# Performance work log

Measured on AMD Instinct MI355X. Metric: run time of the kernel, lower is better.

## Reference

```python
import math
import jax, jax.numpy as jnp
import numpy as np

B, S, D, H, DFF, MEM = 4, 1024, 1024, 16, 4096, 256
HD = D // H  # 64
EPS = 1e-5


def _ln(x, g, b):
    mu = jnp.mean(x, axis=-1, keepdims=True)
    var = jnp.mean(jnp.square(x - mu), axis=-1, keepdims=True)
    return (x - mu) * jax.lax.rsqrt(var + EPS) * g + b


def _rope(x, cos, sin):
    # x: (b, h, s, hd); cos/sin: (>=s, hd//2)
    s = x.shape[2]
    xp = x.reshape(*x.shape[:-1], -1, 2)
    x0, x1 = xp[..., 0], xp[..., 1]
    c = cos[:s][None, None]
    sn = sin[:s][None, None]
    r0 = x0 * c - x1 * sn
    r1 = x0 * sn + x1 * c
    return jnp.stack([r0, r1], axis=-1).reshape(x.shape)


def setup_inputs() -> dict:
    key = jax.random.key(0)
    ks = jax.random.split(key, 16)
    p = lambda k, shape: jax.random.normal(k, shape, dtype=jnp.float32) * 0.02

    tgt = jax.random.normal(ks[0], (B, S, D), dtype=jnp.float32)
    memory = jax.random.normal(ks[1], (B, MEM, D), dtype=jnp.float32)

    # causal additive mask (s, s)
    tgt_mask = jnp.where(jnp.tril(jnp.ones((S, S), bool)), 0.0, -1e9).astype(jnp.float32)

    # RoPE freqs, theta=10000
    inv_freq = 1.0 / (10000.0 ** (np.arange(0, HD, 2, dtype=np.float32) / HD))
    ang = np.arange(S, dtype=np.float32)[:, None] * inv_freq[None, :]
    rope_cos = jnp.asarray(np.cos(ang))
    rope_sin = jnp.asarray(np.sin(ang))

    return {
        "tgt": tgt, "memory": memory, "tgt_mask": tgt_mask,
        "rope_cos": rope_cos, "rope_sin": rope_sin,
        "qkv_w": p(ks[2], (3 * D, D)), "qkv_b": jnp.zeros((3 * D,), jnp.float32),
        "out_w": p(ks[3], (D, D)), "out_b": jnp.zeros((D,), jnp.float32),
        "ca_in_w": p(ks[4], (3 * D, D)), "ca_in_b": jnp.zeros((3 * D,), jnp.float32),
        "ca_out_w": p(ks[5], (D, D)), "ca_out_b": jnp.zeros((D,), jnp.float32),
        "ffn_w1": p(ks[6], (DFF, D)), "ffn_b1": jnp.zeros((DFF,), jnp.float32),
        "ffn_w2": p(ks[7], (D, DFF)), "ffn_b2": jnp.zeros((D,), jnp.float32),
        "ln1_g": jnp.ones((D,), jnp.float32), "ln1_b": jnp.zeros((D,), jnp.float32),
        "ln2_g": jnp.ones((D,), jnp.float32), "ln2_b": jnp.zeros((D,), jnp.float32),
        "ln3_g": jnp.ones((D,), jnp.float32), "ln3_b": jnp.zeros((D,), jnp.float32),
    }


def reference(tgt, memory, tgt_mask, rope_cos, rope_sin,
              qkv_w, qkv_b, out_w, out_b,
              ca_in_w, ca_in_b, ca_out_w, ca_out_b,
              ffn_w1, ffn_b1, ffn_w2, ffn_b2,
              ln1_g, ln1_b, ln2_g, ln2_b, ln3_g, ln3_b):
    b, s, d = tgt.shape
    scale = 1.0 / math.sqrt(HD)

    # ---- self-attention with RoPE ----
    x = _ln(tgt, ln1_g, ln1_b)
    qkv = (x @ qkv_w.T + qkv_b).reshape(b, s, 3, H, HD)
    qkv = jnp.transpose(qkv, (2, 0, 3, 1, 4))  # (3, b, h, s, hd)
    q, k, v = qkv[0], qkv[1], qkv[2]
    q = _rope(q, rope_cos, rope_sin)
    k = _rope(k, rope_cos, rope_sin)
    attn = jnp.einsum('bhqd,bhkd->bhqk', q, k) * scale
    attn = attn + tgt_mask[None, None]
    attn = jax.nn.softmax(attn, axis=-1)
    sa = jnp.einsum('bhqk,bhkd->bhqd', attn, v)
    sa = jnp.transpose(sa, (0, 2, 1, 3)).reshape(b, s, d)
    tgt = tgt + (sa @ out_w.T + out_b)

    # ---- cross-attention (standard MHA, no positional encoding) ----
    x = _ln(tgt, ln2_g, ln2_b)
    wq, wk, wv = jnp.split(ca_in_w, 3, axis=0)
    bq, bk, bv = jnp.split(ca_in_b, 3, axis=0)
    m = memory.shape[1]
    cq = (x @ wq.T + bq).reshape(b, s, H, HD).transpose(0, 2, 1, 3)
    ck = (memory @ wk.T + bk).reshape(b, m, H, HD).transpose(0, 2, 1, 3)
    cv = (memory @ wv.T + bv).reshape(b, m, H, HD).transpose(0, 2, 1, 3)
    cattn = jax.nn.softmax(jnp.einsum('bhqd,bhkd->bhqk', cq, ck) * scale, axis=-1)
    co = jnp.einsum('bhqk,bhkd->bhqd', cattn, cv)
    co = jnp.transpose(co, (0, 2, 1, 3)).reshape(b, s, d)
    tgt = tgt + (co @ ca_out_w.T + ca_out_b)

    # ---- FFN (exact GELU, as torch nn.GELU default) ----
    x = _ln(tgt, ln3_g, ln3_b)
    ff = jax.nn.gelu(x @ ffn_w1.T + ffn_b1, approximate=False) @ ffn_w2.T + ffn_b2
    return tgt + ff
```

## Files before the change

kernel.cpp:

```cpp
#include <hip/hip_runtime.h>
#include <hip/hip_bf16.h>


using bf16 = __hip_bfloat16;
typedef __bf16 bf16x8 __attribute__((ext_vector_type(8)));
typedef float f32x4 __attribute__((ext_vector_type(4)));

static constexpr int Bn = 4, Ssz = 1024, Dm = 1024, Hh = 16, HDd = 64, DFFn = 4096, MEMn = 256;

__device__ inline float bf2f(bf16 x) { return __bfloat162float(x); }
__device__ inline bf16 f2bf(float x) { return __float2bfloat16(x); }

__global__ void detect_kernel(const unsigned* __restrict__ cosw, int* __restrict__ flag) {
  if (threadIdx.x == 0) *flag = (cosw[0] == 0x3F800000u) ? 1 : 0;
}

struct CanonArgs {
  const void* src[23];
  void* dst[23];
  int n[23];
};
__global__ __launch_bounds__(256) void canon_all(CanonArgs a, float* __restrict__ resid,
                                                 const int* __restrict__ flagp) {
  const int seg = blockIdx.y;
  const int n4 = a.n[seg] >> 2;
  if (n4 == 0) return;
  const int fl = *flagp;
  if (fl) {
    const float4* s = (const float4*)a.src[seg];
    bf16* d = (bf16*)a.dst[seg];
    for (int i = blockIdx.x * 256 + threadIdx.x; i < n4; i += gridDim.x * 256) {
      float4 v = s[i];
      bf16 t[4] = {f2bf(v.x), f2bf(v.y), f2bf(v.z), f2bf(v.w)};
      *reinterpret_cast<unsigned long long*>(d + i * 4) =
          *reinterpret_cast<unsigned long long*>(t);
      if (seg == 0) *reinterpret_cast<float4*>(resid + i * 4) = v;
    }
  } else {
    const unsigned long long* s = (const unsigned long long*)a.src[seg];
    unsigned long long* d = (unsigned long long*)a.dst[seg];
    for (int i = blockIdx.x * 256 + threadIdx.x; i < n4; i += gridDim.x * 256) {
      unsigned long long v = s[i];
      d[i] = v;
      if (seg == 0) {
        const unsigned short* u = reinterpret_cast<const unsigned short*>(&v);
        float4 f;
        f.x = __uint_as_float(((unsigned)u[0]) << 16);
        f.y = __uint_as_float(((unsigned)u[1]) << 16);
        f.z = __uint_as_float(((unsigned)u[2]) << 16);
        f.w = __uint_as_float(((unsigned)u[3]) << 16);
        *reinterpret_cast<float4*>(resid + i * 4) = f;
      }
    }
  }
}

__global__ __launch_bounds__(256) void ln_kernel(const float* __restrict__ x,
                                                 const bf16* __restrict__ g,
                                                 const bf16* __restrict__ bb,
                                                 bf16* __restrict__ y) {
  const int row = blockIdx.x;
  const float* xr = x + (size_t)row * Dm;
  const int i0 = threadIdx.x * 4;
  float4 v = *reinterpret_cast<const float4*>(xr + i0);
  float s = v.x + v.y + v.z + v.w;
  float ss = v.x * v.x + v.y * v.y + v.z * v.z + v.w * v.w;
#pragma unroll
  for (int o = 32; o > 0; o >>= 1) {
    s += __shfl_down(s, o);
    ss += __shfl_down(ss, o);
  }
  __shared__ float shs[4], shss[4];
  const int wave = threadIdx.x >> 6, lane = threadIdx.x & 63;
  if (lane == 0) { shs[wave] = s; shss[wave] = ss; }
  __syncthreads();
  s = shs[0] + shs[1] + shs[2] + shs[3];
  ss = shss[0] + shss[1] + shss[2] + shss[3];
  const float mu = s * (1.0f / Dm);
  const float var = fmaxf(ss * (1.0f / Dm) - mu * mu, 0.0f);
  const float rs = rsqrtf(var + 1e-5f);
  bf16* yr = y + (size_t)row * Dm + i0;
  float vv[4] = {v.x, v.y, v.z, v.w};
#pragma unroll
  for (int j = 0; j < 4; ++j)
    yr[j] = f2bf((vv[j] - mu) * rs * bf2f(g[i0 + j]) + bf2f(bb[i0 + j]));
}

__global__ __launch_bounds__(256) void gemm_bt(
    const bf16* __restrict__ A, const bf16* __restrict__ W,
    const bf16* __restrict__ bias, bf16* __restrict__ outB, float* __restrict__ outF,
    const float* __restrict__ residIn, float* __restrict__ residOut,
    const int* __restrict__ flagp, int M, int N, int K, int epi) {
  __shared__ bf16 As[64][40];
  __shared__ bf16 Ws[64][40];
  const int tid = threadIdx.x;
  const int m0 = blockIdx.x * 64, n0 = blockIdx.y * 64;
  const int wave = tid >> 6, lane = tid & 63;
  const int wm = wave >> 1, wn = wave & 1;
  const int quad = lane >> 4, m16 = lane & 15;
  const int lr = tid >> 2, lc = (tid & 3) * 8;

  f32x4 acc[2][2] = {};

  const bf16* Ap = A + (size_t)(m0 + lr) * K + lc;
  const bf16* Wp = W + (size_t)(n0 + lr) * K + lc;
  for (int k0 = 0; k0 < K; k0 += 32) {
    float4 av = *reinterpret_cast<const float4*>(Ap + k0);
    float4 wv = *reinterpret_cast<const float4*>(Wp + k0);
    *reinterpret_cast<float4*>(&As[lr][lc]) = av;
    *reinterpret_cast<float4*>(&Ws[lr][lc]) = wv;
    __syncthreads();
    bf16x8 aF[2], bF[2];
#pragma unroll
    for (int t = 0; t < 2; ++t) {
      aF[t] = *reinterpret_cast<const bf16x8*>(&As[wm * 32 + t * 16 + m16][quad * 8]);
      bF[t] = *reinterpret_cast<const bf16x8*>(&Ws[wn * 32 + t * 16 + m16][quad * 8]);
    }
#pragma unroll
    for (int mt = 0; mt < 2; ++mt)
#pragma unroll
      for (int nt = 0; nt < 2; ++nt)
        acc[mt][nt] = __builtin_amdgcn_mfma_f32_16x16x32_bf16(aF[mt], bF[nt], acc[mt][nt], 0, 0, 0);
    __syncthreads();
  }
  const int fl = (epi == 3) ? *flagp : 0;
#pragma unroll
  for (int mt = 0; mt < 2; ++mt) {
#pragma unroll
    for (int nt = 0; nt < 2; ++nt) {
      const int col = n0 + wn * 32 + nt * 16 + m16;
      const float bv = bf2f(bias[col]);
#pragma unroll
      for (int r = 0; r < 4; ++r) {
        const int row = m0 + wm * 32 + mt * 16 + quad * 4 + r;
        const size_t idx = (size_t)row * N + col;
        float v = acc[mt][nt][r] + bv;
        if (epi == 0) {
          outB[idx] = f2bf(v);
        } else if (epi == 1) {
          outB[idx] = f2bf(0.5f * v * (1.0f + erff(v * 0.70710678118654752f)));
        } else if (epi == 2) {
          residOut[idx] = residIn[idx] + v;
        } else {
          const float rr = residIn[idx] + v;
          if (fl) outF[idx] = rr; else outB[idx] = f2bf(rr);
        }
      }
    }
  }
}

__global__ __launch_bounds__(256) void gemm128(
    const bf16* __restrict__ A, const bf16* __restrict__ W,
    const bf16* __restrict__ bias, bf16* __restrict__ outB, float* __restrict__ outF,
    const float* __restrict__ residIn, float* __restrict__ residOut,
    const int* __restrict__ flagp, int M, int N, int K, int epi) {
  __shared__ bf16 As[128][40];
  __shared__ bf16 Ws[128][40];
  const int tid = threadIdx.x;
  const int wave = tid >> 6, lane = tid & 63;
  const int wm = wave >> 1, wn = wave & 1;
  const int quad = lane >> 4, m16 = lane & 15;
  const int m0 = blockIdx.x * 128, n0 = blockIdx.y * 128;

  const int lr = tid >> 2;
  const int lc = (tid & 3) * 8;
  const bf16* Ap = A + (size_t)(m0 + lr) * K + lc;
  const bf16* Wp = W + (size_t)(n0 + lr) * K + lc;
  const size_t rowOff = (size_t)64 * K;

  f32x4 acc[4][4] = {};

  float4 ax0 = *reinterpret_cast<const float4*>(Ap);
  float4 ax1 = *reinterpret_cast<const float4*>(Ap + rowOff);
  float4 wx0 = *reinterpret_cast<const float4*>(Wp);
  float4 wx1 = *reinterpret_cast<const float4*>(Wp + rowOff);
  float4 ay0 = *reinterpret_cast<const float4*>(Ap + 32);
  float4 ay1 = *reinterpret_cast<const float4*>(Ap + rowOff + 32);
  float4 wy0 = *reinterpret_cast<const float4*>(Wp + 32);
  float4 wy1 = *reinterpret_cast<const float4*>(Wp + rowOff + 32);

  const int nsteps = K >> 5;
  for (int s = 0; s < nsteps; s += 2) {
    *reinterpret_cast<float4*>(&As[lr][lc]) = ax0;
    *reinterpret_cast<float4*>(&As[64 + lr][lc]) = ax1;
    *reinterpret_cast<float4*>(&Ws[lr][lc]) = wx0;
    *reinterpret_cast<float4*>(&Ws[64 + lr][lc]) = wx1;
    __syncthreads();
    if (s + 2 < nsteps) {
      const int k2 = (s + 2) * 32;
      ax0 = *reinterpret_cast<const float4*>(Ap + k2);
      ax1 = *reinterpret_cast<const float4*>(Ap + rowOff + k2);
      wx0 = *reinterpret_cast<const float4*>(Wp + k2);
      wx1 = *reinterpret_cast<const float4*>(Wp + rowOff + k2);
    }
    {
      bf16x8 aF[4], bF[4];
#pragma unroll
      for (int t = 0; t < 4; ++t) {
        aF[t] = *reinterpret_cast<const bf16x8*>(&As[wm * 64 + t * 16 + m16][quad * 8]);
        bF[t] = *reinterpret_cast<const bf16x8*>(&Ws[wn * 64 + t * 16 + m16][quad * 8]);
      }
#pragma unroll
      for (int mt = 0; mt < 4; ++mt)
#pragma unroll
        for (int nt = 0; nt < 4; ++nt)
          acc[mt][nt] = __builtin_amdgcn_mfma_f32_16x16x32_bf16(aF[mt], bF[nt], acc[mt][nt], 0, 0, 0);
    }
    __syncthreads();
    *reinterpret_cast<float4*>(&As[lr][lc]) = ay0;
    *reinterpret_cast<float4*>(&As[64 + lr][lc]) = ay1;
    *reinterpret_cast<float4*>(&Ws[lr][lc]) = wy0;
    *reinterpret_cast<float4*>(&Ws[64 + lr][lc]) = wy1;
    __syncthreads();
    if (s + 3 < nsteps) {
      const int k3 = (s + 3) * 32;
      ay0 = *reinterpret_cast<const float4*>(Ap + k3);
      ay1 = *reinterpret_cast<const float4*>(Ap + rowOff + k3);
      wy0 = *reinterpret_cast<const float4*>(Wp + k3);
      wy1 = *reinterpret_cast<const float4*>(Wp + rowOff + k3);
    }
    {
      bf16x8 aF[4], bF[4];
#pragma unroll
      for (int t = 0; t < 4; ++t) {
        aF[t] = *reinterpret_cast<const bf16x8*>(&As[wm * 64 + t * 16 + m16][quad * 8]);
        bF[t] = *reinterpret_cast<const bf16x8*>(&Ws[wn * 64 + t * 16 + m16][quad * 8]);
      }
#pragma unroll
      for (int mt = 0; mt < 4; ++mt)
#pragma unroll
        for (int nt = 0; nt < 4; ++nt)
          acc[mt][nt] = __builtin_amdgcn_mfma_f32_16x16x32_bf16(aF[mt], bF[nt], acc[mt][nt], 0, 0, 0);
    }
    __syncthreads();
  }
  const int fl = (epi == 3) ? *flagp : 0;
#pragma unroll
  for (int mt = 0; mt < 4; ++mt) {
#pragma unroll
    for (int nt = 0; nt < 4; ++nt) {
      const int col = n0 + wn * 64 + nt * 16 + m16;
      const float bv = bf2f(bias[col]);
#pragma unroll
      for (int r = 0; r < 4; ++r) {
        const int row = m0 + wm * 64 + mt * 16 + quad * 4 + r;
        const size_t idx = (size_t)row * N + col;
        float v = acc[mt][nt][r] + bv;
        if (epi == 0) {
          outB[idx] = f2bf(v);
        } else if (epi == 1) {
          outB[idx] = f2bf(0.5f * v * (1.0f + erff(v * 0.70710678118654752f)));
        } else if (epi == 2) {
          residOut[idx] = residIn[idx] + v;
        } else {
          const float rr = residIn[idx] + v;
          if (fl) outF[idx] = rr; else outB[idx] = f2bf(rr);
        }
      }
    }
  }
}

__global__ __launch_bounds__(256) void rope_kernel(bf16* __restrict__ qkv,
                                                   const bf16* __restrict__ cosb,
                                                   const bf16* __restrict__ sinb) {
  const int idx = blockIdx.x * 256 + threadIdx.x;
  const int i = idx & 31;
  const int h = (idx >> 5) & 15;
  const int r = idx >> 9;
  const int s = r & (Ssz - 1);
  const float c = bf2f(cosb[s * 32 + i]);
  const float sn = bf2f(sinb[s * 32 + i]);
  bf16* base = qkv + (size_t)r * (3 * Dm) + h * 64 + 2 * i;
  float x0 = bf2f(base[0]), x1 = bf2f(base[1]);
  base[0] = f2bf(x0 * c - x1 * sn);
  base[1] = f2bf(x0 * sn + x1 * c);
  x0 = bf2f(base[Dm]); x1 = bf2f(base[Dm + 1]);
  base[Dm] = f2bf(x0 * c - x1 * sn);
  base[Dm + 1] = f2bf(x0 * sn + x1 * c);
}

__global__ __launch_bounds__(256) void attn_mfma(
    const bf16* __restrict__ Qb, const bf16* __restrict__ Kb, const bf16* __restrict__ Vb,
    bf16* __restrict__ Ob, int qStride, int kvStride, int kvLen, int causal, float scale) {
  __shared__ bf16 Ks[64][72];
  __shared__ bf16 Vt[64][72];
  __shared__ bf16 Ps[64][72];
  const int tid = threadIdx.x;
  const int wave = tid >> 6, lane = tid & 63;
  const int quad = lane >> 4, m16 = lane & 15;
  const int b = blockIdx.z, h = blockIdx.y;
  const int q0 = blockIdx.x * 64;
  const int sr = tid >> 2, sc = (tid & 3) * 16;

  {
    const bf16* qp = Qb + (size_t)(b * Ssz + q0 + sr) * qStride + h * 64 + sc;
    float4 a = reinterpret_cast<const float4*>(qp)[0];
    float4 bb2 = reinterpret_cast<const float4*>(qp)[1];
    *reinterpret_cast<float4*>(&Ps[sr][sc]) = a;
    *reinterpret_cast<float4*>(&Ps[sr][sc + 8]) = bb2;
  }
  __syncthreads();
  bf16x8 qf[2];
  qf[0] = *reinterpret_cast<const bf16x8*>(&Ps[wave * 16 + m16][quad * 8]);
  qf[1] = *reinterpret_cast<const bf16x8*>(&Ps[wave * 16 + m16][32 + quad * 8]);

  f32x4 oacc[4] = {};
  float mrow[4], lrow[4];
#pragma unroll
  for (int r = 0; r < 4; ++r) { mrow[r] = -30000.0f; lrow[r] = 0.0f; }

  const int nk = causal ? (q0 + 64) : kvLen;
  for (int kt = 0; kt < nk; kt += 64) {
    {
      const bf16* kp = Kb + (size_t)(b * kvLen + kt + sr) * kvStride + h * 64 + sc;
      float4 k1 = reinterpret_cast<const float4*>(kp)[0];
      float4 k2 = reinterpret_cast<const float4*>(kp)[1];
      *reinterpret_cast<float4*>(&Ks[sr][sc]) = k1;
      *reinterpret_cast<float4*>(&Ks[sr][sc + 8]) = k2;
      const bf16* vp = Vb + (size_t)(b * kvLen + kt + sr) * kvStride + h * 64 + sc;
      float4 v1 = reinterpret_cast<const float4*>(vp)[0];
      float4 v2 = reinterpret_cast<const float4*>(vp)[1];
      const bf16* tv1 = reinterpret_cast<const bf16*>(&v1);
      const bf16* tv2 = reinterpret_cast<const bf16*>(&v2);
#pragma unroll
      for (int j = 0; j < 8; ++j) {
        Vt[sc + j][sr] = tv1[j];
        Vt[sc + 8 + j][sr] = tv2[j];
      }
    }
    __syncthreads();

    f32x4 sacc[4] = {};
#pragma unroll
    for (int nt = 0; nt < 4; ++nt) {
      bf16x8 kf0 = *reinterpret_cast<const bf16x8*>(&Ks[nt * 16 + m16][quad * 8]);
      bf16x8 kf1 = *reinterpret_cast<const bf16x8*>(&Ks[nt * 16 + m16][32 + quad * 8]);
      sacc[nt] = __builtin_amdgcn_mfma_f32_16x16x32_bf16(qf[0], kf0, sacc[nt], 0, 0, 0);
      sacc[nt] = __builtin_amdgcn_mfma_f32_16x16x32_bf16(qf[1], kf1, sacc[nt], 0, 0, 0);
    }
    const bool dmask = (causal != 0) && (kt == q0);
#pragma unroll
    for (int nt = 0; nt < 4; ++nt) {
#pragma unroll
      for (int r = 0; r < 4; ++r) {
        float s = sacc[nt][r] * scale;
        if (dmask && (nt * 16 + m16 > wave * 16 + quad * 4 + r)) s = -30000.0f;
        sacc[nt][r] = s;
      }
    }

#pragma unroll
    for (int r = 0; r < 4; ++r) {
      float mx = fmaxf(fmaxf(sacc[0][r], sacc[1][r]), fmaxf(sacc[2][r], sacc[3][r]));
#pragma unroll
      for (int off = 1; off < 16; off <<= 1) mx = fmaxf(mx, __shfl_xor(mx, off));
      const float mn = fmaxf(mrow[r], mx);
      const float corr = __expf(mrow[r] - mn);
      mrow[r] = mn;
      float psum = 0.0f;
#pragma unroll
      for (int nt = 0; nt < 4; ++nt) {
        const float p = __expf(sacc[nt][r] - mn);
        sacc[nt][r] = p;
        psum += p;
      }
#pragma unroll
      for (int off = 1; off < 16; off <<= 1) psum += __shfl_xor(psum, off);
      lrow[r] = lrow[r] * corr + psum;
#pragma unroll
      for (int nt = 0; nt < 4; ++nt) oacc[nt][r] *= corr;
#pragma unroll
      for (int nt = 0; nt < 4; ++nt)
        Ps[wave * 16 + quad * 4 + r][nt * 16 + m16] = f2bf(sacc[nt][r]);
    }
    bf16x8 pf0 = *reinterpret_cast<const bf16x8*>(&Ps[wave * 16 + m16][quad * 8]);
    bf16x8 pf1 = *reinterpret_cast<const bf16x8*>(&Ps[wave * 16 + m16][32 + quad * 8]);
#pragma unroll
    for (int nt = 0; nt < 4; ++nt) {
      bf16x8 vf0 = *reinterpret_cast<const bf16x8*>(&Vt[nt * 16 + m16][quad * 8]);
      bf16x8 vf1 = *reinterpret_cast<const bf16x8*>(&Vt[nt * 16 + m16][32 + quad * 8]);
      oacc[nt] = __builtin_amdgcn_mfma_f32_16x16x32_bf16(pf0, vf0, oacc[nt], 0, 0, 0);
      oacc[nt] = __builtin_amdgcn_mfma_f32_16x16x32_bf16(pf1, vf1, oacc[nt], 0, 0, 0);
    }
    __syncthreads();
  }

  float inv[4];
#pragma unroll
  for (int r = 0; r < 4; ++r) inv[r] = 1.0f / lrow[r];
#pragma unroll
  for (int r = 0; r < 4; ++r) {
    bf16* op = Ob + (size_t)(b * Ssz + q0 + wave * 16 + quad * 4 + r) * Dm + h * 64 + m16;
#pragma unroll
    for (int nt = 0; nt < 4; ++nt) op[nt * 16] = f2bf(oacc[nt][r] * inv[r]);
  }
}

extern "C" void kernel_launch(void* const* d_in, const int* in_sizes, int n_in,
                              void* d_out, int out_size, void* d_ws, size_t ws_size,
                              hipStream_t stream) {
  char* ws = (char*)d_ws;
  int* flagp   = (int*)ws;
  float* resid = (float*)(ws + (1ull << 20));
  bf16* xln    = (bf16*)(ws + (17ull << 20));
  bf16* aout   = (bf16*)(ws + (25ull << 20));
  bf16* big    = (bf16*)(ws + (33ull << 20));
  size_t off   = (65ull << 20);

  detect_kernel<<<1, 64, 0, stream>>>((const unsigned*)d_in[3], flagp);

  CanonArgs ca;
  bf16* c[23];
  for (int i = 0; i < 23; ++i) {
    if (i == 2) { c[i] = nullptr; ca.src[i] = d_in[i]; ca.dst[i] = nullptr; ca.n[i] = 0; continue; }
    c[i] = (bf16*)(ws + off);
    const int n = in_sizes[i];
    off += ((size_t)n * 2 + 255) & ~(size_t)255;
    ca.src[i] = d_in[i];
    ca.dst[i] = c[i];
    ca.n[i] = n;
  }
  canon_all<<<dim3(256, 23), 256, 0, stream>>>(ca, resid, flagp);

  const bf16 *memory = c[1], *rope_cos = c[3], *rope_sin = c[4];
  const bf16 *qkv_w = c[5], *qkv_b = c[6], *out_w = c[7], *out_b = c[8];
  const bf16 *ca_in_w = c[9], *ca_in_b = c[10], *ca_out_w = c[11], *ca_out_b = c[12];
  const bf16 *ffn_w1 = c[13], *ffn_b1 = c[14], *ffn_w2 = c[15], *ffn_b2 = c[16];
  const bf16 *ln1_g = c[17], *ln1_b = c[18], *ln2_g = c[19], *ln2_b = c[20];
  const bf16 *ln3_g = c[21], *ln3_b = c[22];

  bf16* qb = big;
  bf16* kb = (bf16*)(ws + (41ull << 20));
  bf16* vb = (bf16*)(ws + (43ull << 20));
  bf16* outB = (bf16*)d_out;
  float* outF = (float*)d_out;

  const int ROWS = Bn * Ssz;
  const float scale = 0.125f;

  ln_kernel<<<ROWS, 256, 0, stream>>>(resid, ln1_g, ln1_b, xln);
  gemm128<<<dim3(ROWS / 128, (3 * Dm) / 128), 256, 0, stream>>>(
      xln, qkv_w, qkv_b, big, nullptr, nullptr, nullptr, nullptr, ROWS, 3 * Dm, Dm, 0);
  rope_kernel<<<(ROWS * Hh * (HDd / 2)) / 256, 256, 0, stream>>>(big, rope_cos, rope_sin);
  attn_mfma<<<dim3(Ssz / 64, Hh, Bn), 256, 0, stream>>>(
      big, big + Dm, big + 2 * Dm, aout, 3 * Dm, 3 * Dm, Ssz, 1, scale);
  gemm128<<<dim3(ROWS / 128, Dm / 128), 256, 0, stream>>>(
      aout, out_w, out_b, nullptr, nullptr, resid, resid, nullptr, ROWS, Dm, Dm, 2);

  ln_kernel<<<ROWS, 256, 0, stream>>>(resid, ln2_g, ln2_b, xln);
  gemm128<<<dim3(ROWS / 128, Dm / 128), 256, 0, stream>>>(
      xln, ca_in_w, ca_in_b, qb, nullptr, nullptr, nullptr, nullptr, ROWS, Dm, Dm, 0);
  gemm_bt<<<dim3((Bn * MEMn) / 64, Dm / 64), 256, 0, stream>>>(
      memory, ca_in_w + (size_t)Dm * Dm, ca_in_b + Dm, kb, nullptr, nullptr, nullptr, nullptr,
      Bn * MEMn, Dm, Dm, 0);
  gemm_bt<<<dim3((Bn * MEMn) / 64, Dm / 64), 256, 0, stream>>>(
      memory, ca_in_w + (size_t)2 * Dm * Dm, ca_in_b + 2 * Dm, vb, nullptr, nullptr, nullptr, nullptr,
      Bn * MEMn, Dm, Dm, 0);
  attn_mfma<<<dim3(Ssz / 64, Hh, Bn), 256, 0, stream>>>(
      qb, kb, vb, aout, Dm, Dm, MEMn, 0, scale);
  gemm128<<<dim3(ROWS / 128, Dm / 128), 256, 0, stream>>>(
      aout, ca_out_w, ca_out_b, nullptr, nullptr, resid, resid, nullptr, ROWS, Dm, Dm, 2);

  ln_kernel<<<ROWS, 256, 0, stream>>>(resid, ln3_g, ln3_b, xln);
  gemm128<<<dim3(ROWS / 128, DFFn / 128), 256, 0, stream>>>(
      xln, ffn_w1, ffn_b1, big, nullptr, nullptr, nullptr, nullptr, ROWS, DFFn, Dm, 1);
  gemm128<<<dim3(ROWS / 128, Dm / 128), 256, 0, stream>>>(
      big, ffn_w2, ffn_b2, outB, outF, resid, nullptr, flagp, ROWS, Dm, DFFn, 3);
}
```

Baseline: 584.5 us.

## Load GEMM weight fragments directly from global into registers and swizzle block order

```diff
diff --git a/kernel.cpp b/kernel.cpp
--- a/kernel.cpp
+++ b/kernel.cpp
@@ -156,82 +156,89 @@
     const float* __restrict__ residIn, float* __restrict__ residOut,
     const int* __restrict__ flagp, int M, int N, int K, int epi) {
   __shared__ bf16 As[128][40];
-  __shared__ bf16 Ws[128][40];
   const int tid = threadIdx.x;
   const int wave = tid >> 6, lane = tid & 63;
   const int wm = wave >> 1, wn = wave & 1;
   const int quad = lane >> 4, m16 = lane & 15;
-  const int m0 = blockIdx.x * 128, n0 = blockIdx.y * 128;
+
+  const int numM = gridDim.x;
+  const int lin = blockIdx.y * numM + blockIdx.x;
+  const int grpSz = numM * 8;
+  const int gid = lin / grpSz;
+  const int rem = lin - gid * grpSz;
+  const int m0 = (rem >> 3) * 128;
+  const int n0 = (gid * 8 + (rem & 7)) * 128;
 
   const int lr = tid >> 2;
   const int lc = (tid & 3) * 8;
   const bf16* Ap = A + (size_t)(m0 + lr) * K + lc;
-  const bf16* Wp = W + (size_t)(n0 + lr) * K + lc;
   const size_t rowOff = (size_t)64 * K;
+  const bf16* Wr = W + (size_t)(n0 + wn * 64 + m16) * K + quad * 8;
+  const size_t wK = (size_t)K;
 
   f32x4 acc[4][4] = {};
+  bf16x8 b0[4], b1[4];
 
   float4 ax0 = *reinterpret_cast<const float4*>(Ap);
   float4 ax1 = *reinterpret_cast<const float4*>(Ap + rowOff);
-  float4 wx0 = *reinterpret_cast<const float4*>(Wp);
-  float4 wx1 = *reinterpret_cast<const float4*>(Wp + rowOff);
   float4 ay0 = *reinterpret_cast<const float4*>(Ap + 32);
   float4 ay1 = *reinterpret_cast<const float4*>(Ap + rowOff + 32);
-  float4 wy0 = *reinterpret_cast<const float4*>(Wp + 32);
-  float4 wy1 = *reinterpret_cast<const float4*>(Wp + rowOff + 32);
+#pragma unroll
+  for (int t = 0; t < 4; ++t)
+    b0[t] = *reinterpret_cast<const bf16x8*>(Wr + (size_t)t * 16 * wK);
 
   const int nsteps = K >> 5;
   for (int s = 0; s < nsteps; s += 2) {
     *reinterpret_cast<float4*>(&As[lr][lc]) = ax0;
     *reinterpret_cast<float4*>(&As[64 + lr][lc]) = ax1;
-    *reinterpret_cast<float4*>(&Ws[lr][lc]) = wx0;
-    *reinterpret_cast<float4*>(&Ws[64 + lr][lc]) = wx1;
     __syncthreads();
     if (s + 2 < nsteps) {
       const int k2 = (s + 2) * 32;
       ax0 = *reinterpret_cast<const float4*>(Ap + k2);
       ax1 = *reinterpret_cast<const float4*>(Ap + rowOff + k2);
-      wx0 = *reinterpret_cast<const float4*>(Wp + k2);
-      wx1 = *reinterpret_cast<const float4*>(Wp + rowOff + k2);
     }
     {
-      bf16x8 aF[4], bF[4];
-#pragma unroll
-      for (int t = 0; t < 4; ++t) {
+      const int k1 = (s + 1) * 32;
+#pragma unroll
+      for (int t = 0; t < 4; ++t)
+        b1[t] = *reinterpret_cast<const bf16x8*>(Wr + (size_t)t * 16 * wK + k1);
+    }
+    {
+      bf16x8 aF[4];
+#pragma unroll
+      for (int t = 0; t < 4; ++t)
         aF[t] = *reinterpret_cast<const bf16x8*>(&As[wm * 64 + t * 16 + m16][quad * 8]);
-        bF[t] = *reinterpret_cast<const bf16x8*>(&Ws[wn * 64 + t * 16 + m16][quad * 8]);
-      }
 #pragma unroll
       for (int mt = 0; mt < 4; ++mt)
 #pragma unroll
         for (int nt = 0; nt < 4; ++nt)
-          acc[mt][nt] = __builtin_amdgcn_mfma_f32_16x16x32_bf16(aF[mt], bF[nt], acc[mt][nt], 0, 0, 0);
+          acc[mt][nt] = __builtin_amdgcn_mfma_f32_16x16x32_bf16(aF[mt], b0[nt], acc[mt][nt], 0, 0, 0);
     }
     __syncthreads();
     *reinterpret_cast<float4*>(&As[lr][lc]) = ay0;
     *reinterpret_cast<float4*>(&As[64 + lr][lc]) = ay1;
-    *reinterpret_cast<float4*>(&Ws[lr][lc]) = wy0;
-    *reinterpret_cast<float4*>(&Ws[64 + lr][lc]) = wy1;
     __syncthreads();
     if (s + 3 < nsteps) {
       const int k3 = (s + 3) * 32;
       ay0 = *reinterpret_cast<const float4*>(Ap + k3);
       ay1 = *reinterpret_cast<const float4*>(Ap + rowOff + k3);
-      wy0 = *reinterpret_cast<const float4*>(Wp + k3);
-      wy1 = *reinterpret_cast<const float4*>(Wp + rowOff + k3);
+    }
+    if (s + 2 < nsteps) {
+      const int k2 = (s + 2) * 32;
+#pragma unroll
+      for (int t = 0; t < 4; ++t)
+        b0[t] = *reinterpret_cast<const bf16x8*>(Wr + (size_t)t * 16 * wK + k2);
     }
     {
-      bf16x8 aF[4], bF[4];
-#pragma unroll
-      for (int t = 0; t < 4; ++t) {
+      bf16x8 aF[4];
+#pragma unroll
+      for (int t = 0; t < 4; ++t)
         aF[t] = *reinterpret_cast<const bf16x8*>(&As[wm * 64 + t * 16 + m16][quad * 8]);
-        bF[t] = *reinterpret_cast<const bf16x8*>(&Ws[wn * 64 + t * 16 + m16][quad * 8]);
-      }
 #pragma unroll
       for (int mt = 0; mt < 4; ++mt)
 #pragma unroll
         for (int nt = 0; nt < 4; ++nt)
-          acc[mt][nt] = __builtin_amdgcn_mfma_f32_16x16x32_bf16(aF[mt], bF[nt], acc[mt][nt], 0, 0, 0);
+          acc[mt][nt] = __builtin_amdgcn_mfma_f32_16x16x32_bf16(aF[mt], b1[nt], acc[mt][nt], 0, 0, 0);
     }
     __syncthreads();
   }
```

Measured after the change: 726.4 us. 24.3% more time.
